# Performance work log

Measured on AMD Instinct MI355X. Metric: run time of the kernel, lower is better.

Reference implementation:

```python
import jax, jax.numpy as jnp
import numpy as np

B, S, H = 4, 2048, 1024
NH = 1                     # source code only type-checks with 1 head (see notes)
DH = H // NH               # head dim == hidden size
DT = 32                    # distance_type
LN_EPS = 1e-12


def setup_inputs() -> dict:
    key = jax.random.key(0)
    ks = jax.random.split(key, 12)
    sd = 0.02
    hidden_states = jax.random.normal(ks[0], (B, S, H), dtype=jnp.float32)
    attention_mask = jnp.zeros((B, 1, 1, S), dtype=jnp.float32)
    word_word_relation = jax.random.randint(ks[1], (B, S, S), 0, DT, dtype=jnp.int64)
    dist_emb = sd * jax.random.normal(ks[2], (DT, H), dtype=jnp.float32)
    dist_emb = dist_emb.at[0].set(0.0)  # padding_idx=0
    return {
        "hidden_states": hidden_states,
        "attention_mask": attention_mask,
        "word_word_relation": word_word_relation,
        "Wq": sd * jax.random.normal(ks[3], (H, H), dtype=jnp.float32),
        "bq": jnp.zeros((H,), dtype=jnp.float32),
        "Wk": sd * jax.random.normal(ks[4], (H, H), dtype=jnp.float32),
        "bk": jnp.zeros((H,), dtype=jnp.float32),
        "Wv": sd * jax.random.normal(ks[5], (H, H), dtype=jnp.float32),
        "bv": jnp.zeros((H,), dtype=jnp.float32),
        "dist_emb": dist_emb,
        "Wo": sd * jax.random.normal(ks[6], (H, H), dtype=jnp.float32),
        "bo": jnp.zeros((H,), dtype=jnp.float32),
        "ln_g": jnp.ones((H,), dtype=jnp.float32),
        "ln_b": jnp.zeros((H,), dtype=jnp.float32),
    }


def _split_heads(x):
    # [B,S,H] -> [B,NH,S,DH]
    return x.reshape(B, S, NH, DH).transpose(0, 2, 1, 3)


def reference(hidden_states, attention_mask, word_word_relation, Wq, bq, Wk, bk,
              Wv, bv, dist_emb, Wo, bo, ln_g, ln_b):
    q = _split_heads(hidden_states @ Wq.T + bq)   # [B,NH,S,DH]
    k = _split_heads(hidden_states @ Wk.T + bk)
    v = _split_heads(hidden_states @ Wv.T + bv)

    # raw QK^T scores [B,NH,S,S]
    scores = jnp.einsum('bhqd,bhkd->bhqk', q, k)

    # query . distance_embedding^T : [B,NH,S,DT]
    word_dot_distance = jnp.einsum('bhqd,td->bhqt', q, dist_emb)

    rel = word_word_relation[:, None, :, :]       # [B,1,S,S]
    # gather per-pair distance score along the distance-type axis
    dist_att = jnp.take_along_axis(word_dot_distance, rel, axis=3)  # [B,NH,S,S]
    mask_out = (rel == 1).astype(scores.dtype)    # keep only relation==1 pairs
    dist_att = dist_att * mask_out

    scores = (scores + dist_att) / jnp.sqrt(jnp.asarray(DH, scores.dtype))
    scores = scores + attention_mask              # additive BERT mask
    probs = jax.nn.softmax(scores, axis=-1)       # dropout p=0 -> identity

    ctx = jnp.einsum('bhqk,bhkd->bhqd', probs, v) # [B,NH,S,DH]
    ctx = ctx.transpose(0, 2, 1, 3).reshape(B, S, H)

    # BertSelfOutput: dense -> residual -> LayerNorm
    attn_out = ctx @ Wo.T + bo
    x = attn_out + hidden_states
    mu = jnp.mean(x, axis=-1, keepdims=True)
    var = jnp.mean(jnp.square(x - mu), axis=-1, keepdims=True)
    out = (x - mu) * jax.lax.rsqrt(var + LN_EPS) * ln_g + ln_b
    return out
```

## Files before the change

kernel.cpp:

```cpp
#include <hip/hip_runtime.h>

#define BM 128
#define BN 128
#define BKH 32

typedef __bf16 bf16x8 __attribute__((ext_vector_type(8)));
typedef __bf16 bf16x4 __attribute__((ext_vector_type(4)));
typedef float f32x4 __attribute__((ext_vector_type(4)));
typedef __bf16 bf16_t;

__device__ __forceinline__ void gl_lds16(const void* g, void* l) {
    __builtin_amdgcn_global_load_lds(
        (const __attribute__((address_space(1))) void*)g,
        (__attribute__((address_space(3))) void*)l, 16, 0, 0);
}

__global__ __launch_bounds__(256)
void cvt_kernel(const float* __restrict__ in, bf16_t* __restrict__ out, int n)
{
    const int i = (blockIdx.x * 256 + threadIdx.x) * 4;
    if (i < n) {
        const float4 v = *(const float4*)(in + i);
        bf16x4 o;
        o[0] = (__bf16)v.x; o[1] = (__bf16)v.y;
        o[2] = (__bf16)v.z; o[3] = (__bf16)v.w;
        *(bf16x4*)(out + i) = o;
    }
}

template <int MODE, int SWIZ>
__global__ __launch_bounds__(256)
void gemm_bt(const bf16_t* __restrict__ A, const bf16_t* __restrict__ Bw,
             const float* __restrict__ bias, const float* __restrict__ bias2,
             const float* __restrict__ bias3,
             bf16_t* __restrict__ C, bf16_t* __restrict__ C2,
             int M, int N, int K,
             long long sAz, long long sBz, long long sCz,
             const int* __restrict__ rel, const float* __restrict__ d1,
             const float* __restrict__ resid,
             int Sdim, int DHdim)
{
    const int bz = blockIdx.z;
    const float* bi = bias;
    if (MODE == 0) {
        Bw += (long long)bz * N * K;
        bi = (bz == 0) ? bias : (bz == 1 ? bias2 : bias3);
        if (bz < 2) C += (long long)bz * sCz;
    } else {
        A += (long long)bz * sAz;
        Bw += (long long)bz * sBz;
        C += (long long)bz * sCz;
    }

    int m0, n0;
    if (SWIZ) {
        const int num_n = N / BN;
        const int pid = blockIdx.x;
        const int group = 8 * num_n;
        const int g = pid / group;
        m0 = (g * 8 + (pid % 8)) * BM;
        n0 = ((pid % group) / 8) * BN;
    } else {
        m0 = blockIdx.y * BM;
        n0 = blockIdx.x * BN;
    }
    const int tid = threadIdx.x;
    const int w = tid >> 6;
    const int lane = tid & 63;
    const int wr = w >> 1;
    const int wc = w & 1;
    const int srow = lane >> 2;
    const int scol = (lane & 3) * 8;
    const int frow = lane & 15;
    const int fk = (lane >> 4) * 8;

    __shared__ bf16_t smem[4 * BM * BKH];
    bf16_t* A0 = smem;
    bf16_t* A1 = smem + BM * BKH;
    bf16_t* B0 = smem + 2 * BM * BKH;
    bf16_t* B1 = smem + 3 * BM * BKH;

    f32x4 acc[4][4];
#pragma unroll
    for (int i = 0; i < 4; ++i)
#pragma unroll
        for (int j = 0; j < 4; ++j) acc[i][j] = (f32x4)0.0f;

    for (int k0 = 0; k0 < K; k0 += 2 * BKH) {
#pragma unroll
        for (int i = 0; i < 2; ++i) {
            const int r = i * 64 + w * 16;
            const bf16_t* ga = A + (size_t)(m0 + r + srow) * K + (k0 + scol);
            const bf16_t* gb = Bw + (size_t)(n0 + r + srow) * K + (k0 + scol);
            gl_lds16(ga,        &A0[r * BKH]);
            gl_lds16(ga + BKH,  &A1[r * BKH]);
            gl_lds16(gb,        &B0[r * BKH]);
            gl_lds16(gb + BKH,  &B1[r * BKH]);
        }
        __syncthreads();
#pragma unroll
        for (int h = 0; h < 2; ++h) {
            const bf16_t* Ah = h ? A1 : A0;
            const bf16_t* Bh = h ? B1 : B0;
            bf16x8 af[4], bfv[4];
#pragma unroll
            for (int t = 0; t < 4; ++t) {
                af[t]  = *(const bf16x8*)&Ah[(wr * 64 + t * 16 + frow) * BKH + fk];
                bfv[t] = *(const bf16x8*)&Bh[(wc * 64 + t * 16 + frow) * BKH + fk];
            }
#pragma unroll
            for (int mt = 0; mt < 4; ++mt)
#pragma unroll
                for (int nt = 0; nt < 4; ++nt)
                    acc[mt][nt] = __builtin_amdgcn_mfma_f32_16x16x32_bf16(
                        af[mt], bfv[nt], acc[mt][nt], 0, 0, 0);
        }
        __syncthreads();
    }

    const int crow = (lane >> 4) * 4;
    const int ccol = lane & 15;

    if (MODE == 0 && bz == 2) {
#pragma unroll
        for (int mt = 0; mt < 4; ++mt) {
            const int mb = m0 + wr * 64 + mt * 16 + crow;
#pragma unroll
            for (int nt = 0; nt < 4; ++nt) {
                const int n = n0 + wc * 64 + nt * 16 + ccol;
                const float bv = bi[n];
                const int b = mb >> 11;
                const int s = mb & 2047;
                union { ushort4 u; bf16_t h[4]; } pk;
#pragma unroll
                for (int r = 0; r < 4; ++r) pk.h[r] = (__bf16)(acc[mt][nt][r] + bv);
                *(ushort4*)&C2[(size_t)b * DHdim * Sdim + (size_t)n * Sdim + s] = pk.u;
            }
        }
        return;
    }

    bf16_t* tw = smem + w * (16 * 72);
    const int r0 = lane >> 3;
    const int cseg = (lane & 7) * 8;

    float bv[4];
    if (MODE == 0 || MODE == 4) {
#pragma unroll
        for (int nt = 0; nt < 4; ++nt)
            bv[nt] = bi[n0 + wc * 64 + nt * 16 + ccol];
    }

#pragma unroll
    for (int mt = 0; mt < 4; ++mt) {
#pragma unroll
        for (int nt = 0; nt < 4; ++nt) {
            const float badd = (MODE == 0 || MODE == 4) ? bv[nt] : 0.0f;
#pragma unroll
            for (int r = 0; r < 4; ++r)
                tw[(crow + r) * 72 + nt * 16 + ccol] = (__bf16)(acc[mt][nt][r] + badd);
        }
        bf16x8 va = *(const bf16x8*)&tw[r0 * 72 + cseg];
        bf16x8 vb = *(const bf16x8*)&tw[(r0 + 8) * 72 + cseg];

        const int gm_a = m0 + wr * 64 + mt * 16 + r0;
        const int gm_b = gm_a + 8;
        const int gn = n0 + wc * 64 + cseg;

        if (MODE == 0 || MODE == 3) {
            *(bf16x8*)&C[(size_t)gm_a * N + gn] = va;
            *(bf16x8*)&C[(size_t)gm_b * N + gn] = vb;
        } else if (MODE == 2) {
            const long long ra = ((long long)bz * M + gm_a) * N + gn;
            const long long rb = ((long long)bz * M + gm_b) * N + gn;
            const int4 ra0 = *(const int4*)&rel[ra];
            const int4 ra1 = *(const int4*)&rel[ra + 4];
            const int4 rb0 = *(const int4*)&rel[rb];
            const int4 rb1 = *(const int4*)&rel[rb + 4];
            const float da = d1[(size_t)bz * M + gm_a];
            const float db = d1[(size_t)bz * M + gm_b];
            bf16x8 oa, ob;
            oa[0] = (__bf16)((float)va[0] + (ra0.x == 1 ? da : 0.0f));
            oa[1] = (__bf16)((float)va[1] + (ra0.y == 1 ? da : 0.0f));
            oa[2] = (__bf16)((float)va[2] + (ra0.z == 1 ? da : 0.0f));
            oa[3] = (__bf16)((float)va[3] + (ra0.w == 1 ? da : 0.0f));
            oa[4] = (__bf16)((float)va[4] + (ra1.x == 1 ? da : 0.0f));
            oa[5] = (__bf16)((float)va[5] + (ra1.y == 1 ? da : 0.0f));
            oa[6] = (__bf16)((float)va[6] + (ra1.z == 1 ? da : 0.0f));
            oa[7] = (__bf16)((float)va[7] + (ra1.w == 1 ? da : 0.0f));
            ob[0] = (__bf16)((float)vb[0] + (rb0.x == 1 ? db : 0.0f));
            ob[1] = (__bf16)((float)vb[1] + (rb0.y == 1 ? db : 0.0f));
            ob[2] = (__bf16)((float)vb[2] + (rb0.z == 1 ? db : 0.0f));
            ob[3] = (__bf16)((float)vb[3] + (rb0.w == 1 ? db : 0.0f));
            ob[4] = (__bf16)((float)vb[4] + (rb1.x == 1 ? db : 0.0f));
            ob[5] = (__bf16)((float)vb[5] + (rb1.y == 1 ? db : 0.0f));
            ob[6] = (__bf16)((float)vb[6] + (rb1.z == 1 ? db : 0.0f));
            ob[7] = (__bf16)((float)vb[7] + (rb1.w == 1 ? db : 0.0f));
            *(bf16x8*)&C[(size_t)gm_a * N + gn] = oa;
            *(bf16x8*)&C[(size_t)gm_b * N + gn] = ob;
        } else {
            const float4 xa0 = *(const float4*)&resid[(size_t)gm_a * N + gn];
            const float4 xa1 = *(const float4*)&resid[(size_t)gm_a * N + gn + 4];
            const float4 xb0 = *(const float4*)&resid[(size_t)gm_b * N + gn];
            const float4 xb1 = *(const float4*)&resid[(size_t)gm_b * N + gn + 4];
            bf16x8 oa, ob;
            oa[0] = (__bf16)((float)va[0] + xa0.x);
            oa[1] = (__bf16)((float)va[1] + xa0.y);
            oa[2] = (__bf16)((float)va[2] + xa0.z);
            oa[3] = (__bf16)((float)va[3] + xa0.w);
            oa[4] = (__bf16)((float)va[4] + xa1.x);
            oa[5] = (__bf16)((float)va[5] + xa1.y);
            oa[6] = (__bf16)((float)va[6] + xa1.z);
            oa[7] = (__bf16)((float)va[7] + xa1.w);
            ob[0] = (__bf16)((float)vb[0] + xb0.x);
            ob[1] = (__bf16)((float)vb[1] + xb0.y);
            ob[2] = (__bf16)((float)vb[2] + xb0.z);
            ob[3] = (__bf16)((float)vb[3] + xb0.w);
            ob[4] = (__bf16)((float)vb[4] + xb1.x);
            ob[5] = (__bf16)((float)vb[5] + xb1.y);
            ob[6] = (__bf16)((float)vb[6] + xb1.z);
            ob[7] = (__bf16)((float)vb[7] + xb1.w);
            *(bf16x8*)&C[(size_t)gm_a * N + gn] = oa;
            *(bf16x8*)&C[(size_t)gm_b * N + gn] = ob;
        }
    }
}

__global__ __launch_bounds__(256)
void d1_kernel(const bf16_t* __restrict__ q, const float* __restrict__ de,
               float* __restrict__ d1, int H)
{
    const int row = blockIdx.x * 4 + (threadIdx.x >> 6);
    const int lane = threadIdx.x & 63;
    const bf16_t* qr = q + (size_t)row * H;
    const float* d1r = de + H;
    float s = 0.0f;
    for (int k = lane; k < H; k += 64)
        s += (float)qr[k] * d1r[k];
#pragma unroll
    for (int off = 32; off; off >>= 1) s += __shfl_down(s, off, 64);
    if (lane == 0) d1[row] = s;
}

__global__ __launch_bounds__(256)
void softmax_kernel(bf16_t* __restrict__ sc, const float* __restrict__ mask, int S)
{
    const int row = blockIdx.x;
    const int b = row >> 11;
    bf16_t* p = sc + (size_t)row * S;
    const int tid = threadIdx.x;
    const int w = tid >> 6, lane = tid & 63;
    bf16x8 x = *(const bf16x8*)(p + tid * 8);
    const float4 mk0 = *(const float4*)&mask[(size_t)b * S + tid * 8];
    const float4 mk1 = *(const float4*)&mask[(size_t)b * S + tid * 8 + 4];
    const float mks[8] = {mk0.x, mk0.y, mk0.z, mk0.w, mk1.x, mk1.y, mk1.z, mk1.w};
    float v[8];
    float mx = -1e30f;
#pragma unroll
    for (int j = 0; j < 8; ++j) {
        v[j] = (float)x[j] * 0.03125f + mks[j];
        mx = fmaxf(mx, v[j]);
    }
#pragma unroll
    for (int off = 32; off; off >>= 1) mx = fmaxf(mx, __shfl_xor(mx, off, 64));
    __shared__ float rmax[4], rsum[4];
    if (lane == 0) rmax[w] = mx;
    __syncthreads();
    mx = fmaxf(fmaxf(rmax[0], rmax[1]), fmaxf(rmax[2], rmax[3]));
    float sum = 0.0f;
#pragma unroll
    for (int j = 0; j < 8; ++j) { v[j] = __expf(v[j] - mx); sum += v[j]; }
#pragma unroll
    for (int off = 32; off; off >>= 1) sum += __shfl_xor(sum, off, 64);
    if (lane == 0) rsum[w] = sum;
    __syncthreads();
    sum = rsum[0] + rsum[1] + rsum[2] + rsum[3];
    const float inv = 1.0f / sum;
    bf16x8 o;
#pragma unroll
    for (int j = 0; j < 8; ++j) o[j] = (__bf16)(v[j] * inv);
    *(bf16x8*)(p + tid * 8) = o;
}

__global__ __launch_bounds__(256)
void ln_kernel(const bf16_t* __restrict__ x, const float* __restrict__ gamma,
               const float* __restrict__ beta, float* __restrict__ out)
{
    const int H = 1024;
    const size_t row = blockIdx.x;
    const int tid = threadIdx.x;
    const int w = tid >> 6, lane = tid & 63;
    bf16x4 xv = *(const bf16x4*)(x + row * H + tid * 4);
    float v[4] = {(float)xv[0], (float)xv[1], (float)xv[2], (float)xv[3]};
    float s = 0.0f, s2 = 0.0f;
#pragma unroll
    for (int j = 0; j < 4; ++j) { s += v[j]; s2 += v[j] * v[j]; }
#pragma unroll
    for (int off = 32; off; off >>= 1) {
        s += __shfl_xor(s, off, 64);
        s2 += __shfl_xor(s2, off, 64);
    }
    __shared__ float rs[4], rs2[4];
    if (lane == 0) { rs[w] = s; rs2[w] = s2; }
    __syncthreads();
    s  = rs[0] + rs[1] + rs[2] + rs[3];
    s2 = rs2[0] + rs2[1] + rs2[2] + rs2[3];
    const float mu  = s * (1.0f / H);
    const float var = s2 * (1.0f / H) - mu * mu;
    const float inv = rsqrtf(var + 1e-12f);
    float4 o;
    const int c = tid * 4;
    o.x = (v[0] - mu) * inv * gamma[c + 0] + beta[c + 0];
    o.y = (v[1] - mu) * inv * gamma[c + 1] + beta[c + 1];
    o.z = (v[2] - mu) * inv * gamma[c + 2] + beta[c + 2];
    o.w = (v[3] - mu) * inv * gamma[c + 3] + beta[c + 3];
    *(float4*)(out + row * H + tid * 4) = o;
}

extern "C" void kernel_launch(void* const* d_in, const int* in_sizes, int n_in,
                              void* d_out, int out_size, void* d_ws, size_t ws_size,
                              hipStream_t stream)
{
    constexpr int B = 4, S = 2048, H = 1024;
    const float* hid = (const float*)d_in[0];
    const float* am  = (const float*)d_in[1];
    const int*   rel = (const int*)d_in[2];
    const float* Wq  = (const float*)d_in[3];
    const float* bq  = (const float*)d_in[4];
    const float* Wk  = (const float*)d_in[5];
    const float* bk  = (const float*)d_in[6];
    const float* Wv  = (const float*)d_in[7];
    const float* bv  = (const float*)d_in[8];
    const float* de  = (const float*)d_in[9];
    const float* Wo  = (const float*)d_in[10];
    const float* bo  = (const float*)d_in[11];
    const float* lng = (const float*)d_in[12];
    const float* lnb = (const float*)d_in[13];
    float* out = (float*)d_out;

    char* ws = (char*)d_ws;
    const int n_tok = B * S;
    const size_t MB = 1024 * 1024;
    bf16_t* hidb = (bf16_t*)(ws);
    bf16_t* Wqb  = (bf16_t*)(ws + 16 * MB);
    bf16_t* Wkb  = (bf16_t*)(ws + 18 * MB);
    bf16_t* Wvb  = (bf16_t*)(ws + 20 * MB);
    bf16_t* Wob  = (bf16_t*)(ws + 22 * MB);
    bf16_t* qb   = (bf16_t*)(ws + 24 * MB);
    bf16_t* kb   = (bf16_t*)(ws + 40 * MB);
    bf16_t* vT   = (bf16_t*)(ws + 56 * MB);
    bf16_t* ctx  = (bf16_t*)(ws + 72 * MB);
    bf16_t* sc   = (bf16_t*)(ws + 88 * MB);
    bf16_t* xb   = (bf16_t*)(ws + 88 * MB);
    float*  d1   = (float*)(ws + 120 * MB);

    const dim3 blk(256);
    const int nH2 = H * H;
    cvt_kernel<<<dim3(n_tok * H / 1024), blk, 0, stream>>>(hid, hidb, n_tok * H);
    cvt_kernel<<<dim3(nH2 / 1024), blk, 0, stream>>>(Wq, Wqb, nH2);
    cvt_kernel<<<dim3(nH2 / 1024), blk, 0, stream>>>(Wk, Wkb, nH2);
    cvt_kernel<<<dim3(nH2 / 1024), blk, 0, stream>>>(Wv, Wvb, nH2);
    cvt_kernel<<<dim3(nH2 / 1024), blk, 0, stream>>>(Wo, Wob, nH2);

    gemm_bt<0, 1><<<dim3(64 * 8, 1, 3), blk, 0, stream>>>(
        hidb, Wqb, bq, bk, bv, qb, vT, n_tok, H, H,
        0, 0, (long long)n_tok * H,
        nullptr, nullptr, nullptr, S, H);
    d1_kernel<<<dim3(n_tok / 4), blk, 0, stream>>>(qb, de, d1, H);
    gemm_bt<2, 0><<<dim3(S / BN, S / BM, B), blk, 0, stream>>>(
        qb, kb, nullptr, nullptr, nullptr, sc, nullptr, S, S, H,
        (long long)S * H, (long long)S * H, (long long)S * S,
        rel, d1, nullptr, S, H);
    softmax_kernel<<<dim3(B * S), blk, 0, stream>>>(sc, am, S);
    gemm_bt<3, 1><<<dim3(16 * 8, 1, B), blk, 0, stream>>>(
        sc, vT, nullptr, nullptr, nullptr, ctx, nullptr, S, H, S,
        (long long)S * S, (long long)H * S, (long long)S * H,
        nullptr, nullptr, nullptr, S, H);
    gemm_bt<4, 1><<<dim3(64 * 8, 1, 1), blk, 0, stream>>>(
        ctx, Wob, bo, nullptr, nullptr, xb, nullptr, n_tok, H, H, 0, 0, 0,
        nullptr, nullptr, hid, S, H);
    ln_kernel<<<dim3(n_tok), blk, 0, stream>>>(xb, lng, lnb, out);
}
```

Baseline: 404.2 us.

## Fuse distance bias into softmax, merge conversion kernels, drop GEMM swizzle

Merges the five fp32-to-bf16 conversion launches into one kernel. Moves the query·dist_emb[1] dot product and the relation==1 bias out of a separate d1 kernel and the QK^T GEMM epilogue into the softmax kernel, so the scores GEMM becomes a plain store. It also switches the PV and output GEMMs from the swizzled 1-D grid to a plain 2-D grid. This cuts launches and epilogue work but adds rel loads and a block reduction to each softmax row, and may lose L2 locality from the swizzle.

Measured after the change: 375.2 us. 1.08x faster.

```diff
diff --git a/kernel.cpp b/kernel.cpp
--- a/kernel.cpp
+++ b/kernel.cpp
@@ -16,16 +16,29 @@
 }
 
 __global__ __launch_bounds__(256)
-void cvt_kernel(const float* __restrict__ in, bf16_t* __restrict__ out, int n)
-{
-    const int i = (blockIdx.x * 256 + threadIdx.x) * 4;
-    if (i < n) {
-        const float4 v = *(const float4*)(in + i);
-        bf16x4 o;
-        o[0] = (__bf16)v.x; o[1] = (__bf16)v.y;
-        o[2] = (__bf16)v.z; o[3] = (__bf16)v.w;
-        *(bf16x4*)(out + i) = o;
-    }
+void cvt_all_kernel(const float* __restrict__ hid,
+                    const float* __restrict__ w0, const float* __restrict__ w1,
+                    const float* __restrict__ w2, const float* __restrict__ w3,
+                    bf16_t* __restrict__ hidb, bf16_t* __restrict__ wb)
+{
+    const int bid = blockIdx.x;
+    const float* src;
+    bf16_t* dst;
+    size_t off;
+    if (bid < 8192) {
+        src = hid; dst = hidb; off = (size_t)bid * 1024;
+    } else {
+        const int i = (bid - 8192) >> 10;
+        src = (i == 0) ? w0 : (i == 1) ? w1 : (i == 2) ? w2 : w3;
+        dst = wb + (size_t)i * 1024 * 1024;
+        off = (size_t)((bid - 8192) & 1023) * 1024;
+    }
+    const size_t idx = off + threadIdx.x * 4;
+    const float4 v = *(const float4*)(src + idx);
+    bf16x4 o;
+    o[0] = (__bf16)v.x; o[1] = (__bf16)v.y;
+    o[2] = (__bf16)v.z; o[3] = (__bf16)v.w;
+    *(bf16x4*)(dst + idx) = o;
 }
 
 template <int MODE, int SWIZ>
@@ -36,7 +49,6 @@
              bf16_t* __restrict__ C, bf16_t* __restrict__ C2,
              int M, int N, int K,
              long long sAz, long long sBz, long long sCz,
-             const int* __restrict__ rel, const float* __restrict__ d1,
              const float* __restrict__ resid,
              int Sdim, int DHdim)
 {
@@ -170,34 +182,6 @@
         if (MODE == 0 || MODE == 3) {
             *(bf16x8*)&C[(size_t)gm_a * N + gn] = va;
             *(bf16x8*)&C[(size_t)gm_b * N + gn] = vb;
-        } else if (MODE == 2) {
-            const long long ra = ((long long)bz * M + gm_a) * N + gn;
-            const long long rb = ((long long)bz * M + gm_b) * N + gn;
-            const int4 ra0 = *(const int4*)&rel[ra];
-            const int4 ra1 = *(const int4*)&rel[ra + 4];
-            const int4 rb0 = *(const int4*)&rel[rb];
-            const int4 rb1 = *(const int4*)&rel[rb + 4];
-            const float da = d1[(size_t)bz * M + gm_a];
-            const float db = d1[(size_t)bz * M + gm_b];
-            bf16x8 oa, ob;
-            oa[0] = (__bf16)((float)va[0] + (ra0.x == 1 ? da : 0.0f));
-            oa[1] = (__bf16)((float)va[1] + (ra0.y == 1 ? da : 0.0f));
-            oa[2] = (__bf16)((float)va[2] + (ra0.z == 1 ? da : 0.0f));
-            oa[3] = (__bf16)((float)va[3] + (ra0.w == 1 ? da : 0.0f));
-            oa[4] = (__bf16)((float)va[4] + (ra1.x == 1 ? da : 0.0f));
-            oa[5] = (__bf16)((float)va[5] + (ra1.y == 1 ? da : 0.0f));
-            oa[6] = (__bf16)((float)va[6] + (ra1.z == 1 ? da : 0.0f));
-            oa[7] = (__bf16)((float)va[7] + (ra1.w == 1 ? da : 0.0f));
-            ob[0] = (__bf16)((float)vb[0] + (rb0.x == 1 ? db : 0.0f));
-            ob[1] = (__bf16)((float)vb[1] + (rb0.y == 1 ? db : 0.0f));
-            ob[2] = (__bf16)((float)vb[2] + (rb0.z == 1 ? db : 0.0f));
-            ob[3] = (__bf16)((float)vb[3] + (rb0.w == 1 ? db : 0.0f));
-            ob[4] = (__bf16)((float)vb[4] + (rb1.x == 1 ? db : 0.0f));
-            ob[5] = (__bf16)((float)vb[5] + (rb1.y == 1 ? db : 0.0f));
-            ob[6] = (__bf16)((float)vb[6] + (rb1.z == 1 ? db : 0.0f));
-            ob[7] = (__bf16)((float)vb[7] + (rb1.w == 1 ? db : 0.0f));
-            *(bf16x8*)&C[(size_t)gm_a * N + gn] = oa;
-            *(bf16x8*)&C[(size_t)gm_b * N + gn] = ob;
         } else {
             const float4 xa0 = *(const float4*)&resid[(size_t)gm_a * N + gn];
             const float4 xa1 = *(const float4*)&resid[(size_t)gm_a * N + gn + 4];
@@ -227,43 +211,44 @@
 }
 
 __global__ __launch_bounds__(256)
-void d1_kernel(const bf16_t* __restrict__ q, const float* __restrict__ de,
-               float* __restrict__ d1, int H)
-{
-    const int row = blockIdx.x * 4 + (threadIdx.x >> 6);
-    const int lane = threadIdx.x & 63;
-    const bf16_t* qr = q + (size_t)row * H;
-    const float* d1r = de + H;
-    float s = 0.0f;
-    for (int k = lane; k < H; k += 64)
-        s += (float)qr[k] * d1r[k];
-#pragma unroll
-    for (int off = 32; off; off >>= 1) s += __shfl_down(s, off, 64);
-    if (lane == 0) d1[row] = s;
-}
-
-__global__ __launch_bounds__(256)
-void softmax_kernel(bf16_t* __restrict__ sc, const float* __restrict__ mask, int S)
-{
+void softmax_kernel(bf16_t* __restrict__ sc, const int* __restrict__ rel,
+                    const bf16_t* __restrict__ q, const float* __restrict__ de,
+                    const float* __restrict__ mask)
+{
+    constexpr int S = 2048, H = 1024;
     const int row = blockIdx.x;
     const int b = row >> 11;
-    bf16_t* p = sc + (size_t)row * S;
     const int tid = threadIdx.x;
     const int w = tid >> 6, lane = tid & 63;
-    bf16x8 x = *(const bf16x8*)(p + tid * 8);
+    __shared__ float rd1[4], rmax[4], rsum[4];
+
+    const bf16x4 q4 = *(const bf16x4*)(q + (size_t)row * H + tid * 4);
+    const float4 e4 = *(const float4*)(de + H + tid * 4);
+    float pd = (float)q4[0] * e4.x + (float)q4[1] * e4.y
+             + (float)q4[2] * e4.z + (float)q4[3] * e4.w;
+#pragma unroll
+    for (int off = 32; off; off >>= 1) pd += __shfl_xor(pd, off, 64);
+    if (lane == 0) rd1[w] = pd;
+    __syncthreads();
+    const float d1s = (rd1[0] + rd1[1] + rd1[2] + rd1[3]) * 0.03125f;
+
+    bf16_t* p = sc + (size_t)row * S;
+    const bf16x8 x = *(const bf16x8*)(p + tid * 8);
+    const int4 rl0 = *(const int4*)&rel[(size_t)row * S + tid * 8];
+    const int4 rl1 = *(const int4*)&rel[(size_t)row * S + tid * 8 + 4];
     const float4 mk0 = *(const float4*)&mask[(size_t)b * S + tid * 8];
     const float4 mk1 = *(const float4*)&mask[(size_t)b * S + tid * 8 + 4];
+    const int rls[8] = {rl0.x, rl0.y, rl0.z, rl0.w, rl1.x, rl1.y, rl1.z, rl1.w};
     const float mks[8] = {mk0.x, mk0.y, mk0.z, mk0.w, mk1.x, mk1.y, mk1.z, mk1.w};
     float v[8];
     float mx = -1e30f;
 #pragma unroll
     for (int j = 0; j < 8; ++j) {
-        v[j] = (float)x[j] * 0.03125f + mks[j];
+        v[j] = (float)x[j] * 0.03125f + mks[j] + (rls[j] == 1 ? d1s : 0.0f);
         mx = fmaxf(mx, v[j]);
     }
 #pragma unroll
     for (int off = 32; off; off >>= 1) mx = fmaxf(mx, __shfl_xor(mx, off, 64));
-    __shared__ float rmax[4], rsum[4];
     if (lane == 0) rmax[w] = mx;
     __syncthreads();
     mx = fmaxf(fmaxf(rmax[0], rmax[1]), fmaxf(rmax[2], rmax[3]));
@@ -343,8 +328,6 @@
     const size_t MB = 1024 * 1024;
     bf16_t* hidb = (bf16_t*)(ws);
     bf16_t* Wqb  = (bf16_t*)(ws + 16 * MB);
-    bf16_t* Wkb  = (bf16_t*)(ws + 18 * MB);
-    bf16_t* Wvb  = (bf16_t*)(ws + 20 * MB);
     bf16_t* Wob  = (bf16_t*)(ws + 22 * MB);
     bf16_t* qb   = (bf16_t*)(ws + 24 * MB);
     bf16_t* kb   = (bf16_t*)(ws + 40 * MB);
@@ -352,32 +335,26 @@
     bf16_t* ctx  = (bf16_t*)(ws + 72 * MB);
     bf16_t* sc   = (bf16_t*)(ws + 88 * MB);
     bf16_t* xb   = (bf16_t*)(ws + 88 * MB);
-    float*  d1   = (float*)(ws + 120 * MB);
 
     const dim3 blk(256);
-    const int nH2 = H * H;
-    cvt_kernel<<<dim3(n_tok * H / 1024), blk, 0, stream>>>(hid, hidb, n_tok * H);
-    cvt_kernel<<<dim3(nH2 / 1024), blk, 0, stream>>>(Wq, Wqb, nH2);
-    cvt_kernel<<<dim3(nH2 / 1024), blk, 0, stream>>>(Wk, Wkb, nH2);
-    cvt_kernel<<<dim3(nH2 / 1024), blk, 0, stream>>>(Wv, Wvb, nH2);
-    cvt_kernel<<<dim3(nH2 / 1024), blk, 0, stream>>>(Wo, Wob, nH2);
+    cvt_all_kernel<<<dim3(8192 + 4 * 1024), blk, 0, stream>>>(
+        hid, Wq, Wk, Wv, Wo, hidb, Wqb);
 
     gemm_bt<0, 1><<<dim3(64 * 8, 1, 3), blk, 0, stream>>>(
         hidb, Wqb, bq, bk, bv, qb, vT, n_tok, H, H,
         0, 0, (long long)n_tok * H,
-        nullptr, nullptr, nullptr, S, H);
-    d1_kernel<<<dim3(n_tok / 4), blk, 0, stream>>>(qb, de, d1, H);
-    gemm_bt<2, 0><<<dim3(S / BN, S / BM, B), blk, 0, stream>>>(
+        nullptr, S, H);
+    gemm_bt<3, 0><<<dim3(S / BN, S / BM, B), blk, 0, stream>>>(
         qb, kb, nullptr, nullptr, nullptr, sc, nullptr, S, S, H,
         (long long)S * H, (long long)S * H, (long long)S * S,
-        rel, d1, nullptr, S, H);
-    softmax_kernel<<<dim3(B * S), blk, 0, stream>>>(sc, am, S);
-    gemm_bt<3, 1><<<dim3(16 * 8, 1, B), blk, 0, stream>>>(
+        nullptr, S, H);
+    softmax_kernel<<<dim3(B * S), blk, 0, stream>>>(sc, rel, qb, de, am);
+    gemm_bt<3, 0><<<dim3(H / BN, S / BM, B), blk, 0, stream>>>(
         sc, vT, nullptr, nullptr, nullptr, ctx, nullptr, S, H, S,
         (long long)S * S, (long long)H * S, (long long)S * H,
-        nullptr, nullptr, nullptr, S, H);
-    gemm_bt<4, 1><<<dim3(64 * 8, 1, 1), blk, 0, stream>>>(
+        nullptr, S, H);
+    gemm_bt<4, 0><<<dim3(H / BN, n_tok / BM, 1), blk, 0, stream>>>(
         ctx, Wob, bo, nullptr, nullptr, xb, nullptr, n_tok, H, H, 0, 0, 0,
-        nullptr, nullptr, hid, S, H);
+        hid, S, H);
     ln_kernel<<<dim3(n_tok), blk, 0, stream>>>(xb, lng, lnb, out);
 }
```
